# Optimization experiments

Hardware: AMD Instinct MI355X
Metric: run time of the kernel (lower is better)

The kernel has to match this reference:

```python
import jax, jax.numpy as jnp
import numpy as np

NUM_HEADS = 16
HIDDEN = 2048
HEAD_DIM = HIDDEN // NUM_HEADS


def setup_inputs() -> dict:
    key = jax.random.key(0)
    ks = jax.random.split(key, 9)
    B, S, D = 2, 2048, HIDDEN
    s = 0.02
    return {
        "hidden_states": jax.random.normal(ks[0], (B, S, D), jnp.float32),
        "attention_mask": jnp.ones((B, S), jnp.float32),
        "Wq": jax.random.normal(ks[1], (D, D), jnp.float32) * s,
        "bq": jnp.zeros((D,), jnp.float32),
        "Wk": jax.random.normal(ks[2], (D, D), jnp.float32) * s,
        "bk": jnp.zeros((D,), jnp.float32),
        "Wv": jax.random.normal(ks[3], (D, D), jnp.float32) * s,
        "bv": jnp.zeros((D,), jnp.float32),
        "Wo": jax.random.normal(ks[4], (D, D), jnp.float32) * s,
        "bo": jnp.zeros((D,), jnp.float32),
    }


def _split_heads(x, B, S):
    # [B, S, D] -> [B, H, S, hd]
    return x.reshape(B, S, NUM_HEADS, HEAD_DIM).transpose(0, 2, 1, 3)


def reference(hidden_states, attention_mask, Wq, bq, Wk, bk, Wv, bv, Wo, bo):
    B, S, D = hidden_states.shape
    scale = HEAD_DIM ** -0.5
    # Projections (torch Linear: x @ W.T + b); q scaled as in source
    q = (jnp.einsum('bsd,ed->bse', hidden_states, Wq) + bq) * scale
    k = jnp.einsum('bsd,ed->bse', hidden_states, Wk) + bk
    v = jnp.einsum('bsd,ed->bse', hidden_states, Wv) + bv
    q = _split_heads(q, B, S)
    k = _split_heads(k, B, S)
    v = _split_heads(v, B, S)
    # scores: [B, H, S, S]
    scores = jnp.einsum('bhqd,bhkd->bhqk', q, k)
    # 2D mask path: [B, S] -> additive mask broadcast over heads/query
    add_mask = (1.0 - attention_mask)[:, None, None, :] * jnp.finfo(scores.dtype).min
    scores = scores + add_mask
    attn = jax.nn.softmax(scores, axis=-1)
    out = jnp.einsum('bhqk,bhkd->bhqd', attn, v)
    out = out.transpose(0, 2, 1, 3).reshape(B, S, D)
    out = jnp.einsum('bsd,ed->bse', out, Wo) + bo
    return out
```

## Files before the change

### kernel.cpp

```cpp
#include <hip/hip_runtime.h>

typedef unsigned short u16;
typedef unsigned int   u32;
typedef __attribute__((ext_vector_type(8))) short short8;
typedef __attribute__((ext_vector_type(4))) float f32x4;

#define DEVI static __device__ __forceinline__

DEVI u16 f2bf(float f) {
  u32 u = __float_as_uint(f);
  u32 r = (u + 0x7FFFu + ((u >> 16) & 1u)) >> 16;
  return (u16)r;
}

DEVI void gload_lds16(const void* g, void* l) {
  __builtin_amdgcn_global_load_lds(
      (const __attribute__((address_space(1))) void*)g,
      (__attribute__((address_space(3))) void*)l, 16, 0, 0);
}

__global__ void __launch_bounds__(256) cvt_kernel(const float4* __restrict__ src,
                                                  uint4* __restrict__ dst, int n8) {
  int i = blockIdx.x * 256 + threadIdx.x;
  if (i >= n8) return;
  float4 a = src[2 * i], b = src[2 * i + 1];
  uint4 o;
  o.x = (u32)f2bf(a.x) | ((u32)f2bf(a.y) << 16);
  o.y = (u32)f2bf(a.z) | ((u32)f2bf(a.w) << 16);
  o.z = (u32)f2bf(b.x) | ((u32)f2bf(b.y) << 16);
  o.w = (u32)f2bf(b.z) | ((u32)f2bf(b.w) << 16);
  dst[i] = o;
}

__global__ void __launch_bounds__(256) cvt4_kernel(
    const float4* __restrict__ s0, const float4* __restrict__ s1,
    const float4* __restrict__ s2, const float4* __restrict__ s3,
    uint4* __restrict__ d0, uint4* __restrict__ d1,
    uint4* __restrict__ d2, uint4* __restrict__ d3, int n8) {
  int i = blockIdx.x * 256 + threadIdx.x;
  if (i >= n8) return;
  int seg = blockIdx.y;
  const float4* s = (seg == 0) ? s0 : (seg == 1) ? s1 : (seg == 2) ? s2 : s3;
  uint4* d = (seg == 0) ? d0 : (seg == 1) ? d1 : (seg == 2) ? d2 : d3;
  float4 a = s[2 * i], b = s[2 * i + 1];
  uint4 o;
  o.x = (u32)f2bf(a.x) | ((u32)f2bf(a.y) << 16);
  o.y = (u32)f2bf(a.z) | ((u32)f2bf(a.w) << 16);
  o.z = (u32)f2bf(b.x) | ((u32)f2bf(b.y) << 16);
  o.w = (u32)f2bf(b.z) | ((u32)f2bf(b.w) << 16);
  d[i] = o;
}

template <int MODE>
__global__ void __launch_bounds__(256) gemm_bt(
    const u16* __restrict__ A, const u16* __restrict__ Bw, void* __restrict__ Cp,
    const float* __restrict__ bias0, const float* __restrict__ bias1,
    const float* __restrict__ bias2, int ldc) {
  constexpr int K = 2048;
  __shared__ __align__(16) u16 As[128 * 32];
  __shared__ __align__(16) u16 Bs[128 * 32];
  const int tid = threadIdx.x, w = tid >> 6, l = tid & 63;
  const int wm = w >> 1, wn = w & 1;
  const int bm = blockIdx.x, bn = blockIdx.y;
  const char* Ab = (const char*)(A + (size_t)bm * 128 * K);
  const char* Bb = (const char*)(Bw + (size_t)bn * 128 * K);
  f32x4 acc[4][4] = {};
  for (int kt = 0; kt < K / 32; ++kt) {
#pragma unroll
    for (int q = 0; q < 2; ++q) {
      int byteoff = q * 4096 + w * 1024 + l * 16;
      int row = byteoff >> 6, colb = byteoff & 63;
      gload_lds16(Ab + (size_t)row * (K * 2) + kt * 64 + colb,
                  (char*)As + q * 4096 + w * 1024);
      gload_lds16(Bb + (size_t)row * (K * 2) + kt * 64 + colb,
                  (char*)Bs + q * 4096 + w * 1024);
    }
    __syncthreads();
    short8 af[4], bf[4];
#pragma unroll
    for (int mi = 0; mi < 4; ++mi)
      af[mi] = *(const short8*)((const char*)As + (wm * 64 + mi * 16 + (l & 15)) * 64 + (l >> 4) * 16);
#pragma unroll
    for (int ni = 0; ni < 4; ++ni)
      bf[ni] = *(const short8*)((const char*)Bs + (wn * 64 + ni * 16 + (l & 15)) * 64 + (l >> 4) * 16);
#pragma unroll
    for (int mi = 0; mi < 4; ++mi)
#pragma unroll
      for (int ni = 0; ni < 4; ++ni)
        acc[mi][ni] = __builtin_amdgcn_mfma_f32_16x16x32_bf16(af[mi], bf[ni], acc[mi][ni], 0, 0, 0);
    __syncthreads();
  }
#pragma unroll
  for (int mi = 0; mi < 4; ++mi) {
    int grow = bm * 128 + wm * 64 + mi * 16 + ((l >> 4) << 2);
#pragma unroll
    for (int ni = 0; ni < 4; ++ni) {
      int gcol = bn * 128 + wn * 64 + ni * 16 + (l & 15);
#pragma unroll
      for (int j = 0; j < 4; ++j) {
        float v = acc[mi][ni][j];
        if (MODE == 0) {
          int seg = gcol >> 11;
          const float* bp = (seg == 0) ? bias0 : (seg == 1 ? bias1 : bias2);
          v += bp[gcol & 2047];
          if (seg == 0) v *= 0.08838834764831845f;
          ((u16*)Cp)[(size_t)(grow + j) * ldc + gcol] = f2bf(v);
        } else {
          ((float*)Cp)[(size_t)(grow + j) * ldc + gcol] = v + bias0[gcol];
        }
      }
    }
  }
}

__global__ void __launch_bounds__(256) attn_kernel(const u16* __restrict__ qkv,
                                                   const float* __restrict__ amask,
                                                   u16* __restrict__ ctx) {
  __shared__ __align__(16) char KtB[64 * 256];
  __shared__ __align__(16) char VtB[128 * 128];
  __shared__ __align__(16) char PbB[4][16 * 128];
  const int tid = threadIdx.x, w = tid >> 6, l = tid & 63;
  const int l15 = l & 15, l4 = l >> 4;
  const int qt = blockIdx.x & 31, h = (blockIdx.x >> 5) & 15, b = (int)(blockIdx.x >> 9);
  const int ld = 6144;
  const u16* qp = qkv + (size_t)(b * 2048 + qt * 64 + w * 16 + l15) * ld + h * 128;
  short8 qf[4];
#pragma unroll
  for (int dc = 0; dc < 4; ++dc) qf[dc] = *(const short8*)(qp + dc * 32 + l4 * 8);
  f32x4 o_[8] = {};
  float m_[4], s_[4];
#pragma unroll
  for (int j = 0; j < 4; ++j) { m_[j] = -INFINITY; s_[j] = 0.f; }
  const u16* kbase = qkv + (size_t)b * 2048 * ld + 2048 + h * 128;
  const u16* vbase = qkv + (size_t)b * 2048 * ld + 4096 + h * 128;
  const float* mbase = amask + b * 2048;
  const int kr = tid >> 2, c0 = (tid & 3) * 32;
  const int kb = (tid & 15) * 4, dvb = (tid >> 4) * 8;
  for (int t = 0; t < 32; ++t) {
    const int k0 = t * 64;
    __syncthreads();
    {
      const u16* kg = kbase + (size_t)(k0 + kr) * ld + c0;
      char* drow = KtB + kr * 256;
      const int sw = (kr & 7) << 4;
#pragma unroll
      for (int u = 0; u < 4; ++u)
        *(uint4*)(drow + ((c0 * 2 + u * 16) ^ sw)) = *(const uint4*)(kg + u * 8);
      uint4 vr[4];
#pragma unroll
      for (int r = 0; r < 4; ++r)
        vr[r] = *(const uint4*)(vbase + (size_t)(k0 + kb + r) * ld + dvb);
#pragma unroll
      for (int dvi = 0; dvi < 8; ++dvi) {
        int dv = dvb + dvi;
        u32 lo = (u32)((const u16*)&vr[0])[dvi] | ((u32)((const u16*)&vr[1])[dvi] << 16);
        u32 hi = (u32)((const u16*)&vr[2])[dvi] | ((u32)((const u16*)&vr[3])[dvi] << 16);
        uint2 pk; pk.x = lo; pk.y = hi;
        *(uint2*)(VtB + dv * 128 + ((kb * 2) ^ ((dv & 7) << 4))) = pk;
      }
    }
    __syncthreads();
    f32x4 s[4] = {};
#pragma unroll
    for (int kc = 0; kc < 4; ++kc) {
      const int krow = kc * 16 + l15;
      const char* krp = KtB + krow * 256;
      const int sw = (krow & 7) << 4;
#pragma unroll
      for (int dc = 0; dc < 4; ++dc) {
        short8 kf = *(const short8*)(krp + ((dc * 64 + l4 * 16) ^ sw));
        s[kc] = __builtin_amdgcn_mfma_f32_16x16x32_bf16(qf[dc], kf, s[kc], 0, 0, 0);
      }
    }
#pragma unroll
    for (int kc = 0; kc < 4; ++kc) {
      float mv = mbase[k0 + kc * 16 + l15];
      float am = (1.0f - mv) * -3.402823466e38f;
#pragma unroll
      for (int j = 0; j < 4; ++j) s[kc][j] += am;
    }
    float fct[4], rs[4];
#pragma unroll
    for (int j = 0; j < 4; ++j) {
      float v = fmaxf(fmaxf(s[0][j], s[1][j]), fmaxf(s[2][j], s[3][j]));
      v = fmaxf(v, __shfl_xor(v, 1));
      v = fmaxf(v, __shfl_xor(v, 2));
      v = fmaxf(v, __shfl_xor(v, 4));
      v = fmaxf(v, __shfl_xor(v, 8));
      float mn = fmaxf(m_[j], v);
      fct[j] = __expf(m_[j] - mn);
      m_[j] = mn;
      rs[j] = 0.f;
    }
#pragma unroll
    for (int kc = 0; kc < 4; ++kc) {
      const int kk = kc * 16 + l15;
#pragma unroll
      for (int j = 0; j < 4; ++j) {
        float p = __expf(s[kc][j] - m_[j]);
        rs[j] += p;
        int qq = l4 * 4 + j;
        *(u16*)(PbB[w] + qq * 128 + ((kk * 2) ^ ((qq & 7) << 4))) = f2bf(p);
      }
    }
#pragma unroll
    for (int j = 0; j < 4; ++j) {
      float v = rs[j];
      v += __shfl_xor(v, 1);
      v += __shfl_xor(v, 2);
      v += __shfl_xor(v, 4);
      v += __shfl_xor(v, 8);
      s_[j] = s_[j] * fct[j] + v;
    }
#pragma unroll
    for (int dvc = 0; dvc < 8; ++dvc)
#pragma unroll
      for (int j = 0; j < 4; ++j) o_[dvc][j] *= fct[j];
    short8 pa[2];
    {
      const int swp = (l15 & 7) << 4;
#pragma unroll
      for (int kh = 0; kh < 2; ++kh)
        pa[kh] = *(const short8*)(PbB[w] + l15 * 128 + ((kh * 64 + l4 * 16) ^ swp));
    }
#pragma unroll
    for (int dvc = 0; dvc < 8; ++dvc) {
      const int dv = dvc * 16 + l15;
      const char* vrp = VtB + dv * 128;
      const int swv = (dv & 7) << 4;
#pragma unroll
      for (int kh = 0; kh < 2; ++kh) {
        short8 vf = *(const short8*)(vrp + ((kh * 64 + l4 * 16) ^ swv));
        o_[dvc] = __builtin_amdgcn_mfma_f32_16x16x32_bf16(pa[kh], vf, o_[dvc], 0, 0, 0);
      }
    }
  }
  float inv[4];
#pragma unroll
  for (int j = 0; j < 4; ++j) inv[j] = 1.0f / s_[j];
  u16* crow = ctx + (size_t)(b * 2048 + qt * 64 + w * 16 + l4 * 4) * 2048 + h * 128;
#pragma unroll
  for (int dvc = 0; dvc < 8; ++dvc)
#pragma unroll
    for (int j = 0; j < 4; ++j)
      crow[(size_t)j * 2048 + dvc * 16 + l15] = f2bf(o_[dvc][j] * inv[j]);
}

extern "C" void kernel_launch(void* const* d_in, const int* in_sizes, int n_in,
                              void* d_out, int out_size, void* d_ws, size_t ws_size,
                              hipStream_t stream) {
  const float* hs    = (const float*)d_in[0];
  const float* amask = (const float*)d_in[1];
  const float* Wq    = (const float*)d_in[2];
  const float* bq    = (const float*)d_in[3];
  const float* Wk    = (const float*)d_in[4];
  const float* bk    = (const float*)d_in[5];
  const float* Wv    = (const float*)d_in[6];
  const float* bv    = (const float*)d_in[7];
  const float* Wo    = (const float*)d_in[8];
  const float* bo    = (const float*)d_in[9];
  float* out = (float*)d_out;

  char* ws = (char*)d_ws;
  u16* hiddenB = (u16*)ws;
  u16* wcatB   = (u16*)(ws + 16777216ull);
  u16* woB     = (u16*)(ws + 16777216ull + 25165824ull);
  u16* qkvB    = (u16*)(ws + 16777216ull + 25165824ull + 8388608ull);
  u16* ctxB    = (u16*)(ws + 16777216ull + 25165824ull + 8388608ull + 50331648ull);

  cvt_kernel<<<4096, 256, 0, stream>>>((const float4*)hs, (uint4*)hiddenB, 1048576);
  cvt4_kernel<<<dim3(2048, 4), 256, 0, stream>>>(
      (const float4*)Wq, (const float4*)Wk, (const float4*)Wv, (const float4*)Wo,
      (uint4*)wcatB, (uint4*)(wcatB + 2048 * 2048), (uint4*)(wcatB + 2 * 2048 * 2048),
      (uint4*)woB, 524288);

  gemm_bt<0><<<dim3(32, 48), 256, 0, stream>>>(hiddenB, wcatB, qkvB, bq, bk, bv, 6144);
  attn_kernel<<<1024, 256, 0, stream>>>(qkvB, amask, ctxB);
  gemm_bt<1><<<dim3(32, 16), 256, 0, stream>>>(ctxB, woB, out, bo, nullptr, nullptr, 2048);
}
```

Before: 509.3 us.

## Process 128 queries per attention block, transpose S computation for lane-local softmax

New measurement: 429.1 us. -15.7%, faster.

```diff
diff --git a/kernel.cpp b/kernel.cpp
--- a/kernel.cpp
+++ b/kernel.cpp
@@ -113,24 +113,26 @@
   }
 }
 
-__global__ void __launch_bounds__(256) attn_kernel(const u16* __restrict__ qkv,
-                                                   const float* __restrict__ amask,
-                                                   u16* __restrict__ ctx) {
+__global__ void __launch_bounds__(256, 2) attn_kernel(const u16* __restrict__ qkv,
+                                                      const float* __restrict__ amask,
+                                                      u16* __restrict__ ctx) {
   __shared__ __align__(16) char KtB[64 * 256];
   __shared__ __align__(16) char VtB[128 * 128];
-  __shared__ __align__(16) char PbB[4][16 * 128];
+  __shared__ __align__(16) char PbB[4][2][2048];
   const int tid = threadIdx.x, w = tid >> 6, l = tid & 63;
   const int l15 = l & 15, l4 = l >> 4;
-  const int qt = blockIdx.x & 31, h = (blockIdx.x >> 5) & 15, b = (int)(blockIdx.x >> 9);
+  const int qt = blockIdx.x & 15, h = (blockIdx.x >> 4) & 15, b = (int)(blockIdx.x >> 8);
   const int ld = 6144;
-  const u16* qp = qkv + (size_t)(b * 2048 + qt * 64 + w * 16 + l15) * ld + h * 128;
-  short8 qf[4];
-#pragma unroll
-  for (int dc = 0; dc < 4; ++dc) qf[dc] = *(const short8*)(qp + dc * 32 + l4 * 8);
-  f32x4 o_[8] = {};
-  float m_[4], s_[4];
-#pragma unroll
-  for (int j = 0; j < 4; ++j) { m_[j] = -INFINITY; s_[j] = 0.f; }
+  const int swq = (l15 & 7) << 4;
+  short8 qf[2][4];
+#pragma unroll
+  for (int qg = 0; qg < 2; ++qg) {
+    const u16* qp = qkv + (size_t)(b * 2048 + qt * 128 + w * 32 + qg * 16 + l15) * ld + h * 128;
+#pragma unroll
+    for (int dc = 0; dc < 4; ++dc) qf[qg][dc] = *(const short8*)(qp + dc * 32 + l4 * 8);
+  }
+  f32x4 o_[2][8] = {};
+  float m_[2] = {-INFINITY, -INFINITY}, s_[2] = {0.f, 0.f};
   const u16* kbase = qkv + (size_t)b * 2048 * ld + 2048 + h * 128;
   const u16* vbase = qkv + (size_t)b * 2048 * ld + 4096 + h * 128;
   const float* mbase = amask + b * 2048;
@@ -160,69 +162,84 @@
       }
     }
     __syncthreads();
-    f32x4 s[4] = {};
+    float4 amv[4];
+#pragma unroll
+    for (int kc = 0; kc < 4; ++kc) {
+      float4 mv = *(const float4*)(mbase + k0 + kc * 16 + l4 * 4);
+      amv[kc].x = (1.0f - mv.x) * -3.402823466e38f;
+      amv[kc].y = (1.0f - mv.y) * -3.402823466e38f;
+      amv[kc].z = (1.0f - mv.z) * -3.402823466e38f;
+      amv[kc].w = (1.0f - mv.w) * -3.402823466e38f;
+    }
+    f32x4 sA[2][4];
 #pragma unroll
     for (int kc = 0; kc < 4; ++kc) {
       const int krow = kc * 16 + l15;
       const char* krp = KtB + krow * 256;
       const int sw = (krow & 7) << 4;
-#pragma unroll
-      for (int dc = 0; dc < 4; ++dc) {
-        short8 kf = *(const short8*)(krp + ((dc * 64 + l4 * 16) ^ sw));
-        s[kc] = __builtin_amdgcn_mfma_f32_16x16x32_bf16(qf[dc], kf, s[kc], 0, 0, 0);
-      }
-    }
-#pragma unroll
-    for (int kc = 0; kc < 4; ++kc) {
-      float mv = mbase[k0 + kc * 16 + l15];
-      float am = (1.0f - mv) * -3.402823466e38f;
-#pragma unroll
-      for (int j = 0; j < 4; ++j) s[kc][j] += am;
-    }
-    float fct[4], rs[4];
-#pragma unroll
-    for (int j = 0; j < 4; ++j) {
-      float v = fmaxf(fmaxf(s[0][j], s[1][j]), fmaxf(s[2][j], s[3][j]));
-      v = fmaxf(v, __shfl_xor(v, 1));
-      v = fmaxf(v, __shfl_xor(v, 2));
-      v = fmaxf(v, __shfl_xor(v, 4));
-      v = fmaxf(v, __shfl_xor(v, 8));
-      float mn = fmaxf(m_[j], v);
-      fct[j] = __expf(m_[j] - mn);
-      m_[j] = mn;
-      rs[j] = 0.f;
-    }
-#pragma unroll
-    for (int kc = 0; kc < 4; ++kc) {
-      const int kk = kc * 16 + l15;
-#pragma unroll
-      for (int j = 0; j < 4; ++j) {
-        float p = __expf(s[kc][j] - m_[j]);
-        rs[j] += p;
-        int qq = l4 * 4 + j;
-        *(u16*)(PbB[w] + qq * 128 + ((kk * 2) ^ ((qq & 7) << 4))) = f2bf(p);
-      }
-    }
-#pragma unroll
-    for (int j = 0; j < 4; ++j) {
-      float v = rs[j];
-      v += __shfl_xor(v, 1);
-      v += __shfl_xor(v, 2);
-      v += __shfl_xor(v, 4);
-      v += __shfl_xor(v, 8);
-      s_[j] = s_[j] * fct[j] + v;
-    }
-#pragma unroll
-    for (int dvc = 0; dvc < 8; ++dvc)
-#pragma unroll
-      for (int j = 0; j < 4; ++j) o_[dvc][j] *= fct[j];
-    short8 pa[2];
-    {
-      const int swp = (l15 & 7) << 4;
+      short8 kf[4];
+#pragma unroll
+      for (int dc = 0; dc < 4; ++dc)
+        kf[dc] = *(const short8*)(krp + ((dc * 64 + l4 * 16) ^ sw));
+#pragma unroll
+      for (int qg = 0; qg < 2; ++qg) {
+        f32x4 tacc = {0.f, 0.f, 0.f, 0.f};
+#pragma unroll
+        for (int dc = 0; dc < 4; ++dc)
+          tacc = __builtin_amdgcn_mfma_f32_16x16x32_bf16(kf[dc], qf[qg][dc], tacc, 0, 0, 0);
+        sA[qg][kc] = tacc;
+      }
+    }
+    float fct[2];
+#pragma unroll
+    for (int qg = 0; qg < 2; ++qg) {
+      float pm = -INFINITY;
+#pragma unroll
+      for (int kc = 0; kc < 4; ++kc) {
+        sA[qg][kc][0] += amv[kc].x; sA[qg][kc][1] += amv[kc].y;
+        sA[qg][kc][2] += amv[kc].z; sA[qg][kc][3] += amv[kc].w;
+#pragma unroll
+        for (int j = 0; j < 4; ++j) pm = fmaxf(pm, sA[qg][kc][j]);
+      }
+      pm = fmaxf(pm, __shfl_xor(pm, 16));
+      pm = fmaxf(pm, __shfl_xor(pm, 32));
+      float mn = fmaxf(m_[qg], pm);
+      fct[qg] = __expf(m_[qg] - mn);
+      m_[qg] = mn;
+      float rs = 0.f;
+#pragma unroll
+      for (int kc = 0; kc < 4; ++kc) {
+#pragma unroll
+        for (int j = 0; j < 4; ++j) {
+          float p = __expf(sA[qg][kc][j] - mn);
+          rs += p;
+          sA[qg][kc][j] = p;
+        }
+        u32 lo = (u32)f2bf(sA[qg][kc][0]) | ((u32)f2bf(sA[qg][kc][1]) << 16);
+        u32 hi = (u32)f2bf(sA[qg][kc][2]) | ((u32)f2bf(sA[qg][kc][3]) << 16);
+        uint2 pk; pk.x = lo; pk.y = hi;
+        *(uint2*)(PbB[w][qg] + l15 * 128 + ((kc * 32 + l4 * 8) ^ swq)) = pk;
+      }
+      rs += __shfl_xor(rs, 16);
+      rs += __shfl_xor(rs, 32);
+      s_[qg] = s_[qg] * fct[qg] + rs;
+    }
+#pragma unroll
+    for (int qg = 0; qg < 2; ++qg) {
+      float fq[4];
+#pragma unroll
+      for (int j = 0; j < 4; ++j) fq[j] = __shfl(fct[qg], l4 * 4 + j);
+#pragma unroll
+      for (int dvc = 0; dvc < 8; ++dvc)
+#pragma unroll
+        for (int j = 0; j < 4; ++j) o_[qg][dvc][j] *= fq[j];
+    }
+    short8 pa[2][2];
+#pragma unroll
+    for (int qg = 0; qg < 2; ++qg)
 #pragma unroll
       for (int kh = 0; kh < 2; ++kh)
-        pa[kh] = *(const short8*)(PbB[w] + l15 * 128 + ((kh * 64 + l4 * 16) ^ swp));
-    }
+        pa[qg][kh] = *(const short8*)(PbB[w][qg] + l15 * 128 + ((kh * 64 + l4 * 16) ^ swq));
 #pragma unroll
     for (int dvc = 0; dvc < 8; ++dvc) {
       const int dv = dvc * 16 + l15;
@@ -231,19 +248,25 @@
 #pragma unroll
       for (int kh = 0; kh < 2; ++kh) {
         short8 vf = *(const short8*)(vrp + ((kh * 64 + l4 * 16) ^ swv));
-        o_[dvc] = __builtin_amdgcn_mfma_f32_16x16x32_bf16(pa[kh], vf, o_[dvc], 0, 0, 0);
-      }
-    }
-  }
-  float inv[4];
-#pragma unroll
-  for (int j = 0; j < 4; ++j) inv[j] = 1.0f / s_[j];
-  u16* crow = ctx + (size_t)(b * 2048 + qt * 64 + w * 16 + l4 * 4) * 2048 + h * 128;
-#pragma unroll
-  for (int dvc = 0; dvc < 8; ++dvc)
-#pragma unroll
-    for (int j = 0; j < 4; ++j)
-      crow[(size_t)j * 2048 + dvc * 16 + l15] = f2bf(o_[dvc][j] * inv[j]);
+#pragma unroll
+        for (int qg = 0; qg < 2; ++qg)
+          o_[qg][dvc] = __builtin_amdgcn_mfma_f32_16x16x32_bf16(pa[qg][kh], vf, o_[qg][dvc], 0, 0, 0);
+      }
+    }
+  }
+#pragma unroll
+  for (int qg = 0; qg < 2; ++qg) {
+    float inv = 1.0f / s_[qg];
+    float iq[4];
+#pragma unroll
+    for (int j = 0; j < 4; ++j) iq[j] = __shfl(inv, l4 * 4 + j);
+    u16* crow = ctx + (size_t)(b * 2048 + qt * 128 + w * 32 + qg * 16 + l4 * 4) * 2048 + h * 128;
+#pragma unroll
+    for (int dvc = 0; dvc < 8; ++dvc)
+#pragma unroll
+      for (int j = 0; j < 4; ++j)
+        crow[(size_t)j * 2048 + dvc * 16 + l15] = f2bf(o_[qg][dvc][j] * iq[j]);
+  }
 }
 
 extern "C" void kernel_launch(void* const* d_in, const int* in_sizes, int n_in,
@@ -275,6 +298,6 @@
       (uint4*)woB, 524288);
 
   gemm_bt<0><<<dim3(32, 48), 256, 0, stream>>>(hiddenB, wcatB, qkvB, bq, bk, bv, 6144);
-  attn_kernel<<<1024, 256, 0, stream>>>(qkvB, amask, ctxB);
+  attn_kernel<<<512, 256, 0, stream>>>(qkvB, amask, ctxB);
   gemm_bt<1><<<dim3(32, 16), 256, 0, stream>>>(ctxB, woB, out, bo, nullptr, nullptr, 2048);
 }
```
